# Kernel optimization log

Hardware: AMD Instinct MI355X
Metric: run time of the kernel (lower is better)

Reference implementation:

```python
import jax, jax.numpy as jnp
import numpy as np

ENC_DIM = 256
DEC_DIM = 256
INT_DIM = 256


def setup_inputs() -> dict:
    key = jax.random.key(0)
    k1, k2, k3, k4, k5 = jax.random.split(key, 5)
    B, T = 64, 2048
    encoder_states = jax.random.normal(k1, (B, T, ENC_DIM), dtype=jnp.float32)
    decoder_state = jax.random.normal(k2, (B, DEC_DIM), dtype=jnp.float32)
    s1 = 1.0 / np.sqrt(ENC_DIM)
    s2 = 1.0 / np.sqrt(DEC_DIM)
    s3 = 1.0 / np.sqrt(INT_DIM)
    w1 = jax.random.uniform(k3, (INT_DIM, ENC_DIM), jnp.float32, -s1, s1)
    w2 = jax.random.uniform(k4, (INT_DIM, DEC_DIM), jnp.float32, -s2, s2)
    v = jax.random.uniform(k5, (1, INT_DIM), jnp.float32, -s3, s3)
    return {"encoder_states": encoder_states, "decoder_state": decoder_state,
            "w1": w1, "w2": w2, "v": v}


def reference(encoder_states, decoder_state, w1, w2, v):
    # scores: v @ tanh(W1 e_t + W2 d) for all t at once
    enc_proj = jnp.einsum('bte,ie->bti', encoder_states, w1)      # [B,T,I]
    dec_proj = jnp.einsum('bd,id->bi', decoder_state, w2)          # [B,I]
    scores = jnp.einsum('bti,oi->bt', jnp.tanh(enc_proj + dec_proj[:, None, :]), v)  # [B,T]
    attention_probs = jax.nn.softmax(scores, axis=1)[:, :, None]   # [B,T,1]
    final_context_vec = jnp.sum(attention_probs * encoder_states, axis=1)  # [B,E]
    return final_context_vec, attention_probs
```

## Files before the change

### kernel.cpp

```cpp
#include <hip/hip_runtime.h>
#include <hip/hip_bf16.h>
#include <math.h>

#define Bq 64
#define Tq 2048
#define Eq 256
#define Dq 256
#define Iq 256

using short8  = __attribute__((ext_vector_type(8))) short;
using floatx4 = __attribute__((ext_vector_type(4))) float;

__device__ __forceinline__ float fast_tanh(float x) {
    float e = __expf(2.0f * x);
    return fmaf(-2.0f, __builtin_amdgcn_rcpf(e + 1.0f), 1.0f);
}

__device__ __forceinline__ ushort f2bf(float x) {
    union { __hip_bfloat16 h; ushort u; } c;
    c.h = __float2bfloat16(x);
    return c.u;
}

__global__ __launch_bounds__(256) void prep_kernel(
    const float* __restrict__ w1, ushort* __restrict__ w1sw,
    const float* __restrict__ dec, const float* __restrict__ w2,
    float* __restrict__ dproj)
{
    if (blockIdx.x < 32) {
        const int kc = blockIdx.x;
        const int i  = threadIdx.x;
        const float* src = w1 + i * Eq + kc * 8;
        float4 f0 = *(const float4*)src;
        float4 f1 = *(const float4*)(src + 4);
        ushort u[8] = { f2bf(f0.x), f2bf(f0.y), f2bf(f0.z), f2bf(f0.w),
                        f2bf(f1.x), f2bf(f1.y), f2bf(f1.z), f2bf(f1.w) };
        *(short8*)&w1sw[(kc * 256 + i) * 8] = *(short8*)u;
    } else {
        const int b = blockIdx.x - 32;
        const int i = threadIdx.x;
        __shared__ float dls[Dq];
        dls[i] = dec[b * Dq + i];
        __syncthreads();
        const float* w2r = w2 + i * Dq;
        float acc = 0.f;
        #pragma unroll 8
        for (int d = 0; d < Dq; d += 4) {
            float4 wv = *(const float4*)&w2r[d];
            float4 dv = *(const float4*)&dls[d];
            acc += wv.x * dv.x + wv.y * dv.y + wv.z * dv.z + wv.w * dv.w;
        }
        dproj[b * Iq + i] = acc;
    }
}

__global__ __launch_bounds__(256, 4) void scores_ctx_kernel(
    const float*  __restrict__ enc,
    const ushort* __restrict__ w1sw,
    const float*  __restrict__ v,
    const float*  __restrict__ dproj,
    float* __restrict__ escore,
    float* __restrict__ ctxp,
    float* __restrict__ denomp)
{
    const int b   = blockIdx.y;
    const int bx  = blockIdx.x;
    const int t0  = bx * 64;
    const int tid = threadIdx.x;
    const int w   = tid >> 6;
    const int l   = tid & 63;
    const int l15 = l & 15;
    const int lq  = l >> 4;

    __shared__ float swred[4 * 64];
    __shared__ float redf[4 * 256];

    float vv[4], dd[4];
    #pragma unroll
    for (int ni = 0; ni < 4; ++ni) {
        const int i = w * 64 + ni * 16 + l15;
        vv[ni] = v[i];
        dd[ni] = dproj[b * Iq + i];
    }

    floatx4 acc[4][4];
    #pragma unroll
    for (int mi = 0; mi < 4; ++mi)
        #pragma unroll
        for (int ni = 0; ni < 4; ++ni)
            acc[mi][ni] = (floatx4)0.f;

    const float* encB = enc + ((size_t)b * Tq + t0) * Eq;
    const float*  aRow = encB + (size_t)l15 * Eq + lq * 8;
    const ushort* vb   = w1sw + (w * 64 + l15) * 8 + lq * 2048;

    #pragma unroll
    for (int k0i = 0; k0i < 4; ++k0i) {
        #pragma unroll
        for (int ks = 0; ks < 2; ++ks) {
            short8 af[4];
            #pragma unroll
            for (int mi = 0; mi < 4; ++mi) {
                const float* p = aRow + (size_t)mi * 16 * Eq + k0i * 64 + ks * 32;
                float4 f0 = *(const float4*)p;
                float4 f1 = *(const float4*)(p + 4);
                ushort u[8] = { f2bf(f0.x), f2bf(f0.y), f2bf(f0.z), f2bf(f0.w),
                                f2bf(f1.x), f2bf(f1.y), f2bf(f1.z), f2bf(f1.w) };
                af[mi] = *(short8*)u;
            }
            short8 bfv[4];
            #pragma unroll
            for (int ni = 0; ni < 4; ++ni)
                bfv[ni] = *(const short8*)(vb + (k0i * 8 + ks * 4) * 2048 + ni * 128);

            __builtin_amdgcn_s_setprio(1);
            #pragma unroll
            for (int mi = 0; mi < 4; ++mi)
                #pragma unroll
                for (int ni = 0; ni < 4; ++ni)
                    acc[mi][ni] = __builtin_amdgcn_mfma_f32_16x16x32_bf16(
                        af[mi], bfv[ni], acc[mi][ni], 0, 0, 0);
            __builtin_amdgcn_s_setprio(0);
        }
    }

    float part[4][4];
    #pragma unroll
    for (int mi = 0; mi < 4; ++mi)
        #pragma unroll
        for (int r = 0; r < 4; ++r) part[mi][r] = 0.f;

    #pragma unroll
    for (int ni = 0; ni < 4; ++ni) {
        const float vi = vv[ni];
        const float dp = dd[ni];
        #pragma unroll
        for (int mi = 0; mi < 4; ++mi)
            #pragma unroll
            for (int r = 0; r < 4; ++r)
                part[mi][r] += vi * fast_tanh(acc[mi][ni][r] + dp);
    }

    #pragma unroll
    for (int mi = 0; mi < 4; ++mi)
        #pragma unroll
        for (int r = 0; r < 4; ++r) {
            float x = part[mi][r];
            x += __shfl_xor(x, 1); x += __shfl_xor(x, 2);
            x += __shfl_xor(x, 4); x += __shfl_xor(x, 8);
            part[mi][r] = x;
        }
    if (l15 == 0) {
        #pragma unroll
        for (int mi = 0; mi < 4; ++mi)
            #pragma unroll
            for (int r = 0; r < 4; ++r)
                swred[w * 64 + mi * 16 + lq * 4 + r] = part[mi][r];
    }
    __syncthreads();

    float s = swred[l] + swred[64 + l] + swred[128 + l] + swred[192 + l];
    const float es = __expf(s);
    if (w == 0) {
        escore[(size_t)b * Tq + t0 + l] = es;
        float tot = es;
        tot += __shfl_xor(tot, 1);  tot += __shfl_xor(tot, 2);
        tot += __shfl_xor(tot, 4);  tot += __shfl_xor(tot, 8);
        tot += __shfl_xor(tot, 16); tot += __shfl_xor(tot, 32);
        if (l == 0) denomp[bx * Bq + b] = tot;
    }

    const int el = l * 4;
    float4 a = {0.f, 0.f, 0.f, 0.f};
    #pragma unroll 8
    for (int tt = 0; tt < 16; ++tt) {
        const int t = w * 16 + tt;
        const float pt = __shfl(es, t);
        float4 ev = *(const float4*)&encB[t * Eq + el];
        a.x += pt * ev.x; a.y += pt * ev.y; a.z += pt * ev.z; a.w += pt * ev.w;
    }
    *(float4*)&redf[w * 256 + el] = a;
    __syncthreads();
    if (w == 0) {
        float4 a0 = *(const float4*)&redf[0 * 256 + el];
        float4 a1 = *(const float4*)&redf[1 * 256 + el];
        float4 a2 = *(const float4*)&redf[2 * 256 + el];
        float4 a3 = *(const float4*)&redf[3 * 256 + el];
        float4 o;
        o.x = a0.x + a1.x + a2.x + a3.x;
        o.y = a0.y + a1.y + a2.y + a3.y;
        o.z = a0.z + a1.z + a2.z + a3.z;
        o.w = a0.w + a1.w + a2.w + a3.w;
        *(float4*)&ctxp[((size_t)bx * Bq + b) * Eq + el] = o;
    }
}

__global__ __launch_bounds__(256) void finalize_kernel(
    const float* __restrict__ ctxp, const float* __restrict__ denomp,
    float* __restrict__ probs, float* __restrict__ ctx)
{
    const int b   = blockIdx.x;
    const int tid = threadIdx.x;

    float d = denomp[(tid & 31) * Bq + b];
    d += __shfl_xor(d, 1);  d += __shfl_xor(d, 2);  d += __shfl_xor(d, 4);
    d += __shfl_xor(d, 8);  d += __shfl_xor(d, 16);
    const float inv = 1.0f / d;

    float* prow = probs + (size_t)b * Tq + tid * 8;
    float4 p0 = *(const float4*)(prow + 0);
    float4 p1 = *(const float4*)(prow + 4);
    p0.x *= inv; p0.y *= inv; p0.z *= inv; p0.w *= inv;
    p1.x *= inv; p1.y *= inv; p1.z *= inv; p1.w *= inv;
    *(float4*)(prow + 0) = p0;
    *(float4*)(prow + 4) = p1;

    float s = 0.f;
    #pragma unroll 8
    for (int c = 0; c < 32; ++c)
        s += ctxp[((size_t)c * Bq + b) * Eq + tid];
    ctx[b * Eq + tid] = s * inv;
}

extern "C" void kernel_launch(void* const* d_in, const int* in_sizes, int n_in,
                              void* d_out, int out_size, void* d_ws, size_t ws_size,
                              hipStream_t stream) {
    const float* enc = (const float*)d_in[0];
    const float* dec = (const float*)d_in[1];
    const float* w1  = (const float*)d_in[2];
    const float* w2  = (const float*)d_in[3];
    const float* v   = (const float*)d_in[4];

    float* out   = (float*)d_out;
    float* ctx   = out;
    float* probs = out + Bq * Eq;

    char* ws = (char*)d_ws;
    float*  ctxp   = (float*)ws;
    float*  denomp = (float*)(ws + (32*Bq*Eq)*4);
    float*  dproj  = (float*)(ws + (32*Bq*Eq)*4 + 32*Bq*4);
    ushort* w1sw   = (ushort*)(ws + (32*Bq*Eq)*4 + 32*Bq*4 + Bq*Iq*4);

    prep_kernel<<<dim3(96), dim3(256), 0, stream>>>(w1, w1sw, dec, w2, dproj);
    scores_ctx_kernel<<<dim3(Tq / 64, Bq), dim3(256), 0, stream>>>(
        enc, w1sw, v, dproj, probs, ctxp, denomp);
    finalize_kernel<<<dim3(Bq), dim3(256), 0, stream>>>(ctxp, denomp, probs, ctx);
}
```

Baseline: 247.9 us.

## Stage encoder tiles into LDS with async global_load_lds triple buffering

Encoder rows for the MFMA A operand are now copied into a three-slot shared-memory ring with direct global-to-LDS loads, prefetched one or two K-chunks ahead. A row-XOR swizzle keeps the LDS reads free of bank conflicts. The intent is to overlap HBM latency with MFMA work instead of stalling on per-lane global loads. This adds 48KB of LDS per block, which can lower occupancy below the 4 blocks per CU requested in launch bounds, and the handwritten vmcnt waits are fragile.

```diff
diff --git a/kernel.cpp b/kernel.cpp
--- a/kernel.cpp
+++ b/kernel.cpp
@@ -20,6 +20,12 @@
     union { __hip_bfloat16 h; ushort u; } c;
     c.h = __float2bfloat16(x);
     return c.u;
+}
+
+__device__ __forceinline__ void async_load16(const void* g, void* l) {
+    __builtin_amdgcn_global_load_lds(
+        (const __attribute__((address_space(1))) void*)g,
+        (__attribute__((address_space(3))) void*)l, 16, 0, 0);
 }
 
 __global__ __launch_bounds__(256) void prep_kernel(
@@ -72,8 +78,8 @@
     const int l15 = l & 15;
     const int lq  = l >> 4;
 
+    __shared__ alignas(16) float Af[3][64 * 64];
     __shared__ float swred[4 * 64];
-    __shared__ float redf[4 * 256];
 
     float vv[4], dd[4];
     #pragma unroll
@@ -82,6 +88,8 @@
         vv[ni] = v[i];
         dd[ni] = dproj[b * Iq + i];
     }
+    asm volatile("s_waitcnt vmcnt(0)" ::: "memory");
+    __builtin_amdgcn_sched_barrier(0);
 
     floatx4 acc[4][4];
     #pragma unroll
@@ -91,37 +99,70 @@
             acc[mi][ni] = (floatx4)0.f;
 
     const float* encB = enc + ((size_t)b * Tq + t0) * Eq;
-    const float*  aRow = encB + (size_t)l15 * Eq + lq * 8;
-    const ushort* vb   = w1sw + (w * 64 + l15) * 8 + lq * 2048;
+
+    const int rS = w * 4 + lq;
+    const int cS = l15 ^ rS;
+    #define STAGE(kt, buf)                                                   \
+        _Pragma("unroll")                                                    \
+        for (int q = 0; q < 4; ++q) {                                        \
+            const int r = q * 16 + rS;                                       \
+            async_load16(encB + (size_t)r * Eq + (kt) * 64 + cS * 4,         \
+                         &Af[buf][q * 1024 + w * 256]);                      \
+        }
+
+    STAGE(0, 0);
+    STAGE(1, 1);
+    asm volatile("s_waitcnt vmcnt(4)" ::: "memory");
+    __builtin_amdgcn_sched_barrier(0);
+
+    const ushort* vb = w1sw + (w * 64 + l15) * 8 + lq * 2048;
 
     #pragma unroll
     for (int k0i = 0; k0i < 4; ++k0i) {
-        #pragma unroll
-        for (int ks = 0; ks < 2; ++ks) {
-            short8 af[4];
+        const int kbuf = k0i % 3;
+        __builtin_amdgcn_s_barrier();
+
+        short8 bfv[2][4];
+        #pragma unroll
+        for (int ks = 0; ks < 2; ++ks)
+            #pragma unroll
+            for (int ni = 0; ni < 4; ++ni)
+                bfv[ks][ni] = *(const short8*)(vb + (k0i * 8 + ks * 4) * 2048 + ni * 128);
+        __builtin_amdgcn_sched_barrier(0);
+
+        if (k0i == 0) { STAGE(2, 2); }
+        if (k0i == 1) { STAGE(3, 0); }
+        __builtin_amdgcn_sched_barrier(0);
+
+        short8 af[2][4];
+        #pragma unroll
+        for (int ks = 0; ks < 2; ++ks)
             #pragma unroll
             for (int mi = 0; mi < 4; ++mi) {
-                const float* p = aRow + (size_t)mi * 16 * Eq + k0i * 64 + ks * 32;
-                float4 f0 = *(const float4*)p;
-                float4 f1 = *(const float4*)(p + 4);
+                const int rr = mi * 16 + l15;
+                const int s0 = (ks * 8 + lq * 2) ^ l15;
+                const int s1 = s0 ^ 1;
+                float4 f0 = *(const float4*)&Af[kbuf][rr * 64 + s0 * 4];
+                float4 f1 = *(const float4*)&Af[kbuf][rr * 64 + s1 * 4];
                 ushort u[8] = { f2bf(f0.x), f2bf(f0.y), f2bf(f0.z), f2bf(f0.w),
                                 f2bf(f1.x), f2bf(f1.y), f2bf(f1.z), f2bf(f1.w) };
-                af[mi] = *(short8*)u;
+                af[ks][mi] = *(short8*)u;
             }
-            short8 bfv[4];
-            #pragma unroll
-            for (int ni = 0; ni < 4; ++ni)
-                bfv[ni] = *(const short8*)(vb + (k0i * 8 + ks * 4) * 2048 + ni * 128);
-
-            __builtin_amdgcn_s_setprio(1);
+
+        if (k0i < 2) { asm volatile("s_waitcnt vmcnt(4)" ::: "memory"); }
+        else         { asm volatile("s_waitcnt vmcnt(0)" ::: "memory"); }
+        __builtin_amdgcn_sched_barrier(0);
+
+        __builtin_amdgcn_s_setprio(1);
+        #pragma unroll
+        for (int ks = 0; ks < 2; ++ks)
             #pragma unroll
             for (int mi = 0; mi < 4; ++mi)
                 #pragma unroll
                 for (int ni = 0; ni < 4; ++ni)
                     acc[mi][ni] = __builtin_amdgcn_mfma_f32_16x16x32_bf16(
-                        af[mi], bfv[ni], acc[mi][ni], 0, 0, 0);
-            __builtin_amdgcn_s_setprio(0);
-        }
+                        af[ks][mi], bfv[ks][ni], acc[mi][ni], 0, 0, 0);
+        __builtin_amdgcn_s_setprio(0);
     }
 
     float part[4][4];
@@ -179,6 +220,7 @@
         float4 ev = *(const float4*)&encB[t * Eq + el];
         a.x += pt * ev.x; a.y += pt * ev.y; a.z += pt * ev.z; a.w += pt * ev.w;
     }
+    float* redf = (float*)&Af[0][0];
     *(float4*)&redf[w * 256 + el] = a;
     __syncthreads();
     if (w == 0) {
```

After: 226.4 us. 8.7% less time.

## Stage encoder tiles through double-buffered LDS with cooperative coalesced loads

Applied to the files above, without the earlier changes.

Encoder rows for the MFMA A operand are now loaded cooperatively by the whole block as coalesced float4 rows, converted to bf16 once, and written into a double-buffered LDS tile. Each k-step reads its A fragments from LDS while the next global chunk is in flight. Before this, every wave loaded and converted its own strided fragments from global memory. The change adds LDS usage and barriers, and lowers the occupancy hint from 4 to 3 blocks per CU.

```diff
diff --git a/kernel.cpp b/kernel.cpp
--- a/kernel.cpp
+++ b/kernel.cpp
@@ -54,7 +54,7 @@
     }
 }
 
-__global__ __launch_bounds__(256, 4) void scores_ctx_kernel(
+__global__ __launch_bounds__(256, 3) void scores_ctx_kernel(
     const float*  __restrict__ enc,
     const ushort* __restrict__ w1sw,
     const float*  __restrict__ v,
@@ -72,6 +72,7 @@
     const int l15 = l & 15;
     const int lq  = l >> 4;
 
+    __shared__ alignas(16) ushort As[2][64 * 72];
     __shared__ float swred[4 * 64];
     __shared__ float redf[4 * 256];
 
@@ -91,38 +92,71 @@
             acc[mi][ni] = (floatx4)0.f;
 
     const float* encB = enc + ((size_t)b * Tq + t0) * Eq;
-    const float*  aRow = encB + (size_t)l15 * Eq + lq * 8;
-    const ushort* vb   = w1sw + (w * 64 + l15) * 8 + lq * 2048;
-
-    #pragma unroll
-    for (int k0i = 0; k0i < 4; ++k0i) {
-        #pragma unroll
-        for (int ks = 0; ks < 2; ++ks) {
-            short8 af[4];
-            #pragma unroll
-            for (int mi = 0; mi < 4; ++mi) {
-                const float* p = aRow + (size_t)mi * 16 * Eq + k0i * 64 + ks * 32;
-                float4 f0 = *(const float4*)p;
-                float4 f1 = *(const float4*)(p + 4);
-                ushort u[8] = { f2bf(f0.x), f2bf(f0.y), f2bf(f0.z), f2bf(f0.w),
-                                f2bf(f1.x), f2bf(f1.y), f2bf(f1.z), f2bf(f1.w) };
-                af[mi] = *(short8*)u;
-            }
-            short8 bfv[4];
-            #pragma unroll
-            for (int ni = 0; ni < 4; ++ni)
-                bfv[ni] = *(const short8*)(vb + (k0i * 8 + ks * 4) * 2048 + ni * 128);
-
-            __builtin_amdgcn_s_setprio(1);
-            #pragma unroll
-            for (int mi = 0; mi < 4; ++mi)
-                #pragma unroll
-                for (int ni = 0; ni < 4; ++ni)
-                    acc[mi][ni] = __builtin_amdgcn_mfma_f32_16x16x32_bf16(
-                        af[mi], bfv[ni], acc[mi][ni], 0, 0, 0);
-            __builtin_amdgcn_s_setprio(0);
+    const int srow = tid >> 4;
+    const int sc4  = (tid & 15) * 4;
+
+    #define LOADC(kt, st)                                                     \
+        _Pragma("unroll")                                                     \
+        for (int r = 0; r < 4; ++r)                                           \
+            st[r] = *(const float4*)&encB[(srow + 16 * r) * Eq + (kt) * 64 + sc4];
+    #define CVTW(st, buf)                                                     \
+        _Pragma("unroll")                                                     \
+        for (int r = 0; r < 4; ++r) {                                         \
+            ushort4 u;                                                        \
+            u.x = f2bf(st[r].x); u.y = f2bf(st[r].y);                         \
+            u.z = f2bf(st[r].z); u.w = f2bf(st[r].w);                         \
+            *(ushort4*)&As[buf][(srow + 16 * r) * 72 + sc4] = u;              \
         }
-    }
+    #define BARRIER()                                                         \
+        asm volatile("s_waitcnt lgkmcnt(0)" ::: "memory");                    \
+        __builtin_amdgcn_s_barrier();                                         \
+        __builtin_amdgcn_sched_barrier(0);
+
+    const ushort* vb = w1sw + (w * 64 + l15) * 8 + lq * 2048;
+
+    #define KSTEP(k, cur, LOADNEXT, CVTPREV)                                  \
+    {                                                                         \
+        short8 bfv[2][4];                                                     \
+        _Pragma("unroll")                                                     \
+        for (int ks = 0; ks < 2; ++ks)                                        \
+            _Pragma("unroll")                                                 \
+            for (int ni = 0; ni < 4; ++ni)                                    \
+                bfv[ks][ni] = *(const short8*)(vb + ((k) * 8 + ks * 4) * 2048 \
+                                               + ni * 128);                   \
+        LOADNEXT                                                              \
+        _Pragma("unroll")                                                     \
+        for (int ks = 0; ks < 2; ++ks) {                                      \
+            const int kloc = ks * 32 + lq * 8;                                \
+            short8 af[4];                                                     \
+            _Pragma("unroll")                                                 \
+            for (int mi = 0; mi < 4; ++mi)                                    \
+                af[mi] = *(const short8*)&As[cur][(mi * 16 + l15) * 72 + kloc];\
+            __builtin_amdgcn_s_setprio(1);                                    \
+            _Pragma("unroll")                                                 \
+            for (int mi = 0; mi < 4; ++mi)                                    \
+                _Pragma("unroll")                                             \
+                for (int ni = 0; ni < 4; ++ni)                                \
+                    acc[mi][ni] = __builtin_amdgcn_mfma_f32_16x16x32_bf16(    \
+                        af[mi], bfv[ks][ni], acc[mi][ni], 0, 0, 0);           \
+            __builtin_amdgcn_s_setprio(0);                                    \
+        }                                                                     \
+        CVTPREV                                                               \
+    }
+
+    float4 s0[4], s1[4];
+    LOADC(0, s0);
+    LOADC(1, s1);
+    CVTW(s0, 0);
+    BARRIER();
+
+    KSTEP(0, 0, LOADC(2, s0);, CVTW(s1, 1); BARRIER();)
+    KSTEP(1, 1, LOADC(3, s1);, CVTW(s0, 0); BARRIER();)
+    KSTEP(2, 0, ;,             CVTW(s1, 1); BARRIER();)
+    KSTEP(3, 1, ;,             ;)
+
+    #undef KSTEP
+    #undef LOADC
+    #undef CVTW
 
     float part[4][4];
     #pragma unroll
```

After: 218.3 us. -12.0%, faster.
